# Optimization experiments

Hardware: AMD Instinct MI355X
Metric: run time of the kernel (lower is better)

## Reference

```python
import jax, jax.numpy as jnp
import numpy as np

NEG_INF = -1e8  # matches neg_inf in the numba kernel


def setup_inputs() -> dict:
    key = jax.random.key(0)
    k1, k2 = jax.random.split(key)
    B, N, M, S = 128, 256, 256, 3
    theta = jax.random.normal(k1, (B, N, M, S), dtype=jnp.float32)
    A = jax.random.normal(k2, (B, N, M, S, S), dtype=jnp.float32)
    # state transition offsets: match, insert, delete
    pos = jnp.array([[-1, -1], [-1, 0], [0, -1]], dtype=jnp.int64)
    return {"theta": theta, "A": A, "pos": pos}


def _forward(theta, A, pos):
    # theta: [B,N,M,S], A: [B,N,M,S,S], pos: [S,2] with entries in {(-1,-1),(-1,0),(0,-1)}
    B, N, M, S = theta.shape
    # map each state k to its source cell: 0 -> V[i-1,j-1], 1 -> V[i-1,j], 2 -> V[i,j-1]
    idx = jnp.where(pos[:, 0] == -1,
                    jnp.where(pos[:, 1] == -1, 0, 1), 2)  # [S]

    # v_prev holds row i-1, columns 0..M. Row 0: V[0,0,:]=0, rest = NEG_INF.
    v0 = jnp.full((B, M + 1, S), NEG_INF, theta.dtype)
    v0 = v0.at[:, 0, :].set(0.0)

    def row_step(v_prev, row):
        theta_r, A_r = row                               # [M,B,S], [M,B,S,S]
        prev_jm1 = jnp.swapaxes(v_prev[:, :M], 0, 1)     # V[i-1, j-1] : [M,B,S]
        prev_j = jnp.swapaxes(v_prev[:, 1:], 0, 1)       # V[i-1, j]   : [M,B,S]

        def col_step(v_left, xs):
            pjm1, pj, th, a = xs                         # [B,S],[B,S],[B,S],[B,S,S]
            cand = jnp.stack([pjm1, pj, v_left], axis=0) # [3,B,S]
            src = cand[idx]                              # [S,B,S]: source V per state k
            scores = jnp.swapaxes(src, 0, 1) + a         # [B,S(k),S(L)]
            v_new = jax.nn.logsumexp(scores, axis=-1) + th  # [B,S]
            return v_new, v_new

        v_left0 = jnp.full((B, S), NEG_INF, theta.dtype)  # column 0 boundary
        _, v_row = jax.lax.scan(col_step, v_left0, (prev_jm1, prev_j, theta_r, A_r))
        v_row = jnp.swapaxes(v_row, 0, 1)                # [B,M,S]
        v_prev_new = jnp.concatenate(
            [jnp.full((B, 1, S), NEG_INF, theta.dtype), v_row], axis=1)
        return v_prev_new, None

    theta_t = jnp.transpose(theta, (1, 2, 0, 3))  # [N,M,B,S]
    A_t = jnp.transpose(A, (1, 2, 0, 3, 4))       # [N,M,B,S,S]
    v_last, _ = jax.lax.scan(row_step, v0, (theta_t, A_t))
    # terminal log-partition: logsumexp over states at cell (N, M)
    return jax.nn.logsumexp(v_last[:, M, :], axis=-1)  # [B]


def reference(theta, A, pos):
    return _forward(theta, A, pos)
```

## Files before the change

### kernel.cpp

```cpp
#include <hip/hip_runtime.h>


#define NEG_INF -1.0e8f

constexpr int Nr = 256;
constexpr int Mc = 256;
constexpr int Ss = 3;

__device__ __forceinline__ float lae2(float x, float y) {
    float m = fmaxf(x, y);
    float d = fminf(x, y) - m;
    return m + __logf(1.0f + __expf(d));
}

__device__ __forceinline__ float lse3(float x0, float x1, float x2) {
    float m = fmaxf(x0, fmaxf(x1, x2));
    return m + __logf(__expf(x0 - m) + __expf(x1 - m) + __expf(x2 - m));
}

__global__ __launch_bounds__(256, 1)
void ForwardDecoder_kernel(const float* __restrict__ theta,
                           const float* __restrict__ A,
                           float* __restrict__ out) {
    const int b    = blockIdx.x;
    const int t    = threadIdx.x;
    const int lane = t & 63;
    const int wave = t >> 6;

    __shared__ float vbuf0[(Mc + 1) * Ss];
    __shared__ float vbuf1[(Mc + 1) * Ss];
    __shared__ float wtA[4], wtB[4];

    for (int k = t; k < (Mc + 1) * Ss; k += 256) vbuf0[k] = (k < Ss) ? 0.0f : NEG_INF;
    __syncthreads();

    float* cur = vbuf0;
    float* nxt = vbuf1;

    const float* thBase = theta + (size_t)b * Nr * Mc * Ss;
    const float* ABase  = A     + (size_t)b * Nr * Mc * Ss * Ss;

    float rTh[3], rA[9], rNb[8];
    float pTh[3], pA[9], pNb[8];

    auto load_row = [&](int ri, float* Th, float* Aa, float* Nb) {
        const float* thp = thBase + (size_t)ri * Mc * Ss + t * Ss;
        const float* ap  = ABase  + (size_t)ri * Mc * Ss * Ss + t * Ss * Ss;
        Th[0] = thp[0]; Th[1] = thp[1]; Th[2] = thp[2];
        #pragma unroll
        for (int k = 0; k < 9; ++k) Aa[k] = ap[k];
        if (t > 0) {
            const float* thn = thp - Ss;
            const float* an  = ap - Ss * Ss;
            Nb[0] = thn[0]; Nb[1] = thn[1];
            Nb[2] = an[0];  Nb[3] = an[1];  Nb[4] = an[2];
            Nb[5] = an[3];  Nb[6] = an[4];  Nb[7] = an[5];
        } else {
            #pragma unroll
            for (int k = 0; k < 8; ++k) Nb[k] = NEG_INF;
        }
    };

    load_row(0, rTh, rA, rNb);

    for (int i = 0; i < Nr; ++i) {
        if (i + 1 < Nr) load_row(i + 1, pTh, pA, pNb);

        float pdm0 = NEG_INF, pdm1 = NEG_INF, pdm2 = NEG_INF;
        if (t > 0) { pdm0 = cur[(t-1)*3+0]; pdm1 = cur[(t-1)*3+1]; pdm2 = cur[(t-1)*3+2]; }
        float pd0 = cur[t*3+0],     pd1 = cur[t*3+1],     pd2 = cur[t*3+2];
        float pu0 = cur[(t+1)*3+0], pu1 = cur[(t+1)*3+1], pu2 = cur[(t+1)*3+2];

        float v0 = rTh[0] + lse3(pd0 + rA[0], pd1 + rA[1], pd2 + rA[2]);
        float v1 = rTh[1] + lse3(pu0 + rA[3], pu1 + rA[4], pu2 + rA[5]);

        float nv0, nv1;
        if (t > 0) {
            nv0 = rNb[0] + lse3(pdm0 + rNb[2], pdm1 + rNb[3], pdm2 + rNb[4]);
            nv1 = rNb[1] + lse3(pd0  + rNb[5], pd1  + rNb[6], pd2  + rNb[7]);
        } else { nv0 = NEG_INF; nv1 = NEG_INF; }

        float a  = rTh[2] + rA[8];
        float bb = rTh[2] + lae2(nv0 + rA[6], nv1 + rA[7]);

        #pragma unroll
        for (int d = 1; d < 64; d <<= 1) {
            float ao = __shfl_up(a, d, 64);
            float bo = __shfl_up(bb, d, 64);
            if (lane >= d) {
                bb = lae2(a + bo, bb);
                a  = ao + a;
            }
        }
        if (lane == 63) { wtA[wave] = a; wtB[wave] = bb; }
        __syncthreads();

        if (wave > 0) {
            float ca = wtA[0], cb = wtB[0];
            #pragma unroll
            for (int w = 1; w < 3; ++w) {
                if (w < wave) {
                    cb = lae2(wtA[w] + cb, wtB[w]);
                    ca = ca + wtA[w];
                }
            }
            bb = lae2(a + cb, bb);
            a  = ca + a;
        }
        float v2 = lae2(a + NEG_INF, bb);

        nxt[(t+1)*3+0] = v0; nxt[(t+1)*3+1] = v1; nxt[(t+1)*3+2] = v2;
        if (t == 0) { nxt[0] = NEG_INF; nxt[1] = NEG_INF; nxt[2] = NEG_INF; }
        __syncthreads();

        float* tmp = cur; cur = nxt; nxt = tmp;
        #pragma unroll
        for (int k = 0; k < 3; ++k) rTh[k] = pTh[k];
        #pragma unroll
        for (int k = 0; k < 9; ++k) rA[k] = pA[k];
        #pragma unroll
        for (int k = 0; k < 8; ++k) rNb[k] = pNb[k];
    }

    if (t == 0) {
        out[b] = lse3(cur[Mc*3+0], cur[Mc*3+1], cur[Mc*3+2]);
    }
}

extern "C" void kernel_launch(void* const* d_in, const int* in_sizes, int n_in,
                              void* d_out, int out_size, void* d_ws, size_t ws_size,
                              hipStream_t stream) {
    const float* theta = (const float*)d_in[0];
    const float* A     = (const float*)d_in[1];
    float* out = (float*)d_out;

    const int B = in_sizes[0] / (Nr * Mc * Ss);
    ForwardDecoder_kernel<<<B, 256, 0, stream>>>(theta, A, out);
}
```

Baseline: 875.4 us.

## Use one wavefront per batch with four columns per lane and register-resident rows

Each batch row is now handled by a single 64-lane wavefront, with every lane owning four consecutive columns. The previous row's values stay in registers and neighbours are exchanged with shuffles instead of LDS. A serial in-lane prefix is followed by a wave-level scan, which removes both __syncthreads per row and the cross-wave combine. Loads become float4 vectors with double-buffered row prefetch. In exchange there are fewer threads per block, so less parallelism to hide latency, and register pressure is higher.

```diff
diff --git a/kernel.cpp b/kernel.cpp
--- a/kernel.cpp
+++ b/kernel.cpp
@@ -5,7 +5,6 @@
 
 constexpr int Nr = 256;
 constexpr int Mc = 256;
-constexpr int Ss = 3;
 
 __device__ __forceinline__ float lae2(float x, float y) {
     float m = fmaxf(x, y);
@@ -18,112 +17,106 @@
     return m + __logf(__expf(x0 - m) + __expf(x1 - m) + __expf(x2 - m));
 }
 
-__global__ __launch_bounds__(256, 1)
+__global__ __launch_bounds__(64, 1)
 void ForwardDecoder_kernel(const float* __restrict__ theta,
                            const float* __restrict__ A,
                            float* __restrict__ out) {
-    const int b    = blockIdx.x;
-    const int t    = threadIdx.x;
-    const int lane = t & 63;
-    const int wave = t >> 6;
+    const int b = blockIdx.x;
+    const int L = threadIdx.x;
 
-    __shared__ float vbuf0[(Mc + 1) * Ss];
-    __shared__ float vbuf1[(Mc + 1) * Ss];
-    __shared__ float wtA[4], wtB[4];
+    const float* thp = theta + ((size_t)b * Nr * Mc + 4 * L) * 3;
+    const float* ap  = A     + ((size_t)b * Nr * Mc + 4 * L) * 9;
 
-    for (int k = t; k < (Mc + 1) * Ss; k += 256) vbuf0[k] = (k < Ss) ? 0.0f : NEG_INF;
-    __syncthreads();
+    float pv0[4], pv1[4], pv2[4];
+    #pragma unroll
+    for (int j = 0; j < 4; ++j) { pv0[j] = NEG_INF; pv1[j] = NEG_INF; pv2[j] = NEG_INF; }
 
-    float* cur = vbuf0;
-    float* nxt = vbuf1;
+    float cTh[12], cAa[36];
+    float nTh[12], nAa[36];
 
-    const float* thBase = theta + (size_t)b * Nr * Mc * Ss;
-    const float* ABase  = A     + (size_t)b * Nr * Mc * Ss * Ss;
-
-    float rTh[3], rA[9], rNb[8];
-    float pTh[3], pA[9], pNb[8];
-
-    auto load_row = [&](int ri, float* Th, float* Aa, float* Nb) {
-        const float* thp = thBase + (size_t)ri * Mc * Ss + t * Ss;
-        const float* ap  = ABase  + (size_t)ri * Mc * Ss * Ss + t * Ss * Ss;
-        Th[0] = thp[0]; Th[1] = thp[1]; Th[2] = thp[2];
+    auto load_row = [&](int r, float* Th, float* Aa) {
+        const float4* t4 = reinterpret_cast<const float4*>(thp + (size_t)r * Mc * 3);
         #pragma unroll
-        for (int k = 0; k < 9; ++k) Aa[k] = ap[k];
-        if (t > 0) {
-            const float* thn = thp - Ss;
-            const float* an  = ap - Ss * Ss;
-            Nb[0] = thn[0]; Nb[1] = thn[1];
-            Nb[2] = an[0];  Nb[3] = an[1];  Nb[4] = an[2];
-            Nb[5] = an[3];  Nb[6] = an[4];  Nb[7] = an[5];
-        } else {
-            #pragma unroll
-            for (int k = 0; k < 8; ++k) Nb[k] = NEG_INF;
+        for (int q = 0; q < 3; ++q) {
+            float4 v = t4[q];
+            Th[4*q+0] = v.x; Th[4*q+1] = v.y; Th[4*q+2] = v.z; Th[4*q+3] = v.w;
+        }
+        const float4* a4 = reinterpret_cast<const float4*>(ap + (size_t)r * Mc * 9);
+        #pragma unroll
+        for (int q = 0; q < 9; ++q) {
+            float4 v = a4[q];
+            Aa[4*q+0] = v.x; Aa[4*q+1] = v.y; Aa[4*q+2] = v.z; Aa[4*q+3] = v.w;
         }
     };
 
-    load_row(0, rTh, rA, rNb);
+    auto compute_row = [&](int r, const float* Th, const float* Aa) {
+        float bl0 = __shfl_up(pv0[3], 1, 64);
+        float bl1 = __shfl_up(pv1[3], 1, 64);
+        float bl2 = __shfl_up(pv2[3], 1, 64);
+        if (L == 0) {
+            float bv = (r == 0) ? 0.0f : NEG_INF;
+            bl0 = bv; bl1 = bv; bl2 = bv;
+        }
 
-    for (int i = 0; i < Nr; ++i) {
-        if (i + 1 < Nr) load_row(i + 1, pTh, pA, pNb);
+        float v0[4], v1[4];
+        #pragma unroll
+        for (int j = 0; j < 4; ++j) {
+            float d0 = (j == 0) ? bl0 : pv0[j-1];
+            float d1 = (j == 0) ? bl1 : pv1[j-1];
+            float d2 = (j == 0) ? bl2 : pv2[j-1];
+            const float* aj = &Aa[9*j];
+            v0[j] = Th[3*j+0] + lse3(d0 + aj[0], d1 + aj[1], d2 + aj[2]);
+            v1[j] = Th[3*j+1] + lse3(pv0[j] + aj[3], pv1[j] + aj[4], pv2[j] + aj[5]);
+        }
 
-        float pdm0 = NEG_INF, pdm1 = NEG_INF, pdm2 = NEG_INF;
-        if (t > 0) { pdm0 = cur[(t-1)*3+0]; pdm1 = cur[(t-1)*3+1]; pdm2 = cur[(t-1)*3+2]; }
-        float pd0 = cur[t*3+0],     pd1 = cur[t*3+1],     pd2 = cur[t*3+2];
-        float pu0 = cur[(t+1)*3+0], pu1 = cur[(t+1)*3+1], pu2 = cur[(t+1)*3+2];
+        float lx0 = __shfl_up(v0[3], 1, 64);
+        float lx1 = __shfl_up(v1[3], 1, 64);
 
-        float v0 = rTh[0] + lse3(pd0 + rA[0], pd1 + rA[1], pd2 + rA[2]);
-        float v1 = rTh[1] + lse3(pu0 + rA[3], pu1 + rA[4], pu2 + rA[5]);
+        float pa[4], pb[4];
+        #pragma unroll
+        for (int j = 0; j < 4; ++j) {
+            float n0 = (j == 0) ? lx0 : v0[j-1];
+            float n1 = (j == 0) ? lx1 : v1[j-1];
+            if (L == 0 && j == 0) { n0 = NEG_INF; n1 = NEG_INF; }
+            const float* aj = &Aa[9*j];
+            float a  = Th[3*j+2] + aj[8];
+            float bb = Th[3*j+2] + lae2(n0 + aj[6], n1 + aj[7]);
+            if (j == 0) { pa[0] = a; pb[0] = bb; }
+            else        { pa[j] = pa[j-1] + a; pb[j] = lae2(a + pb[j-1], bb); }
+        }
 
-        float nv0, nv1;
-        if (t > 0) {
-            nv0 = rNb[0] + lse3(pdm0 + rNb[2], pdm1 + rNb[3], pdm2 + rNb[4]);
-            nv1 = rNb[1] + lse3(pd0  + rNb[5], pd1  + rNb[6], pd2  + rNb[7]);
-        } else { nv0 = NEG_INF; nv1 = NEG_INF; }
+        float SA = pa[3], SB = pb[3];
+        #pragma unroll
+        for (int d = 1; d < 64; d <<= 1) {
+            float ao = __shfl_up(SA, d, 64);
+            float bo = __shfl_up(SB, d, 64);
+            if (L >= d) {
+                SB = lae2(SA + bo, SB);
+                SA = ao + SA;
+            }
+        }
+        float eA = __shfl_up(SA, 1, 64);
+        float eB = __shfl_up(SB, 1, 64);
+        float xL = (L == 0) ? NEG_INF : lae2(eA + NEG_INF, eB);
 
-        float a  = rTh[2] + rA[8];
-        float bb = rTh[2] + lae2(nv0 + rA[6], nv1 + rA[7]);
+        float v2[4];
+        #pragma unroll
+        for (int j = 0; j < 4; ++j) v2[j] = lae2(pa[j] + xL, pb[j]);
 
         #pragma unroll
-        for (int d = 1; d < 64; d <<= 1) {
-            float ao = __shfl_up(a, d, 64);
-            float bo = __shfl_up(bb, d, 64);
-            if (lane >= d) {
-                bb = lae2(a + bo, bb);
-                a  = ao + a;
-            }
+        for (int j = 0; j < 4; ++j) { pv0[j] = v0[j]; pv1[j] = v1[j]; pv2[j] = v2[j]; }
+
+        if (r == Nr - 1 && L == 63) {
+            out[b] = lse3(v0[3], v1[3], v2[3]);
         }
-        if (lane == 63) { wtA[wave] = a; wtB[wave] = bb; }
-        __syncthreads();
+    };
 
-        if (wave > 0) {
-            float ca = wtA[0], cb = wtB[0];
-            #pragma unroll
-            for (int w = 1; w < 3; ++w) {
-                if (w < wave) {
-                    cb = lae2(wtA[w] + cb, wtB[w]);
-                    ca = ca + wtA[w];
-                }
-            }
-            bb = lae2(a + cb, bb);
-            a  = ca + a;
-        }
-        float v2 = lae2(a + NEG_INF, bb);
-
-        nxt[(t+1)*3+0] = v0; nxt[(t+1)*3+1] = v1; nxt[(t+1)*3+2] = v2;
-        if (t == 0) { nxt[0] = NEG_INF; nxt[1] = NEG_INF; nxt[2] = NEG_INF; }
-        __syncthreads();
-
-        float* tmp = cur; cur = nxt; nxt = tmp;
-        #pragma unroll
-        for (int k = 0; k < 3; ++k) rTh[k] = pTh[k];
-        #pragma unroll
-        for (int k = 0; k < 9; ++k) rA[k] = pA[k];
-        #pragma unroll
-        for (int k = 0; k < 8; ++k) rNb[k] = pNb[k];
-    }
-
-    if (t == 0) {
-        out[b] = lse3(cur[Mc*3+0], cur[Mc*3+1], cur[Mc*3+2]);
+    load_row(0, cTh, cAa);
+    for (int r = 0; r < Nr; r += 2) {
+        if (r + 1 < Nr) load_row(r + 1, nTh, nAa);
+        compute_row(r, cTh, cAa);
+        if (r + 2 < Nr) load_row(r + 2, cTh, cAa);
+        if (r + 1 < Nr) compute_row(r + 1, nTh, nAa);
     }
 }
 
@@ -134,6 +127,6 @@
     const float* A     = (const float*)d_in[1];
     float* out = (float*)d_out;
 
-    const int B = in_sizes[0] / (Nr * Mc * Ss);
-    ForwardDecoder_kernel<<<B, 256, 0, stream>>>(theta, A, out);
+    const int B = in_sizes[0] / (Nr * Mc * 3);
+    ForwardDecoder_kernel<<<B, 64, 0, stream>>>(theta, A, out);
 }
```

Measured after the change: 845.3 us. 1.04x faster.
